# Performance work log

Hardware: AMD Instinct MI355X
Metric: run time of the kernel (lower is better)

The kernel has to match this reference:

```python
import jax, jax.numpy as jnp
import numpy as np

PS = 16          # patch size
NFREQ = 2        # PatchExtractor Fourier frequencies -> 4 + 8*F = 20 channels
E = 8            # num experts
CAP_FACTOR = 1.25


def _pos_feats(h, w, ps, F=NFREQ, dtype=jnp.float32):
    """Fourier positional features per patch pixel: [h*w, 4+8F, ps, ps]."""
    H, W = h * ps, w * ps
    r = jnp.arange(h, dtype=dtype)
    c = jnp.arange(w, dtype=dtype)
    i = jnp.arange(ps, dtype=dtype)
    j = jnp.arange(ps, dtype=dtype)
    gy = (r[:, None, None, None] * ps + i[None, None, :, None]) / H
    gx = (c[None, :, None, None] * ps + j[None, None, None, :]) / W
    pcy = (r[:, None, None, None] + 0.5) / h
    pcx = (c[None, :, None, None] + 0.5) / w
    gy, gx, pcy, pcx = [jnp.broadcast_to(t, (h, w, ps, ps)) for t in (gy, gx, pcy, pcx)]
    feats = [gx, gy, pcx, pcy]
    for f in range(F):
        s = (2.0 ** f) * 2.0 * jnp.pi
        for t in (gx, gy, pcx, pcy):
            feats += [jnp.sin(s * t), jnp.cos(s * t)]
    out = jnp.stack(feats, 0)                       # [4+8F, h, w, ps, ps]
    return out.transpose(1, 2, 0, 3, 4).reshape(h * w, 4 + 8 * F, ps, ps)


def setup_inputs() -> dict:
    key = jax.random.key(0)
    ks = jax.random.split(key, 5)
    X = jax.random.normal(ks[0], (16, 3, 256, 256), jnp.float32)
    expert_w = jax.random.normal(ks[1], (E, 8, 3, 3, 3), jnp.float32) * 0.1   # [E, Cout, Cin, kh, kw]
    expert_b = jnp.zeros((E, 8), jnp.float32)
    gate_w = jax.random.normal(ks[2], (E, 23), jnp.float32) * 0.1             # 1x1 gate conv, mean-pooled
    gate_b = jnp.zeros((E,), jnp.float32)
    lin_w = jax.random.normal(ks[3], (512, 1000), jnp.float32) * 0.02
    lin_b = jnp.zeros((1000,), jnp.float32)
    return dict(X=X, expert_w=expert_w, expert_b=expert_b, gate_w=gate_w,
                gate_b=gate_b, lin_w=lin_w, lin_b=lin_b)


def reference(X, expert_w, expert_b, gate_w, gate_b, lin_w, lin_b):
    B, C, H, W = X.shape
    h, w = H // PS, W // PS
    P = h * w
    N = B * P
    Ccap = int(np.ceil(N * CAP_FACTOR / E))

    # 1. patch extraction: [B,C,H,W] -> [N, C, ps, ps]
    Xp = X.reshape(B, C, h, PS, w, PS).transpose(0, 2, 4, 1, 3, 5).reshape(N, C, PS, PS)

    # patch coords = patch pixels + Fourier positional channels -> [N, C+20, ps, ps]
    pos = _pos_feats(h, w, PS, dtype=X.dtype)
    coords = jnp.concatenate([Xp, jnp.tile(pos, (B, 1, 1, 1))], axis=1)

    # 2. router: 1x1 conv + global mean pool -> logits [N, E]; top-1 capacity routing
    logits = jnp.einsum('nchw,ec->ne', coords, gate_w) / (PS * PS) + gate_b
    probs = jax.nn.softmax(logits, axis=-1)
    e_idx = jnp.argmax(probs, axis=-1)                         # [N] expert choice
    one_hot = jax.nn.one_hot(e_idx, E, dtype=jnp.int32)
    c_idx = jnp.sum(jnp.cumsum(one_hot, axis=0) * one_hot, axis=-1) - 1  # rank within expert
    valid = c_idx < Ccap
    gates = jnp.take_along_axis(probs, e_idx[:, None], axis=1)[:, 0] * valid.astype(probs.dtype)

    # 3. dispatch: scatter patches into per-expert capacity buffers (slot Ccap = dump)
    slot = jnp.where(valid, c_idx, Ccap)
    buf = jnp.zeros((E, Ccap + 1, C, PS, PS), X.dtype).at[e_idx, slot].set(Xp)
    expert_in = buf[:, :Ccap]                                  # [E, Ccap, C, ps, ps]

    # 4. per-expert conv 3x3 + bias + ReLU
    def run_expert(inp, wgt, b):
        y = jax.lax.conv_general_dilated(inp, wgt, (1, 1), 'SAME')
        return jax.nn.relu(y + b[None, :, None, None])

    yout = jax.vmap(run_expert)(expert_in, expert_w, expert_b)  # [E, Ccap, Cout, ps, ps]
    Cout = yout.shape[2]

    # 5. combine: gather each patch's expert output, weighted by gate
    out_n = gates[:, None, None, None] * yout[e_idx, jnp.minimum(c_idx, Ccap - 1)]

    # reassemble patches into full image
    img = out_n.reshape(B, h, w, Cout, PS, PS).transpose(0, 3, 1, 4, 2, 5).reshape(B, Cout, H, W)

    # switch-style aux loss: E * sum_e f_e * p_e
    f_e = jnp.mean(one_hot.astype(probs.dtype) * valid[:, None].astype(probs.dtype), axis=0)
    p_e = jnp.mean(probs, axis=0)
    aux_loss = E * jnp.sum(f_e * p_e)

    # head: adaptive avg pool to 8x8, flatten, linear
    pooled = img.reshape(B, Cout, 8, H // 8, 8, W // 8).mean(axis=(3, 5))
    feat = pooled.reshape(B, -1)
    logits_cls = feat @ lin_w + lin_b
    return logits_cls, aux_loss
```

## Files before the change

kernel.cpp:

```cpp
#include <hip/hip_runtime.h>
#include <math.h>

#define CCAP 640
#define TWO_PI 6.28318530717958647692f

__global__ __launch_bounds__(256) void k_fused(const float* __restrict__ X,
        const float* __restrict__ gw, const float* __restrict__ gb,
        const float* __restrict__ ew, const float* __restrict__ eb,
        int* __restrict__ eidx, float* __restrict__ ptop,
        float* __restrict__ pspart, float* __restrict__ snc)
{
    int tid = threadIdx.x;
    int wave = tid >> 6, lane = tid & 63;
    int n = blockIdx.x * 4 + wave;
    int b = n >> 8, p = n & 255, pr = p >> 4, pc = p & 15;
    int i = lane >> 2, q = lane & 3;

    __shared__ float pb[4][8];

    float4 px[3];
    #pragma unroll
    for (int c = 0; c < 3; ++c)
        px[c] = *(const float4*)(X +
            ((size_t)(b * 3 + c) * 256 + pr * 16 + i) * 256 + pc * 16 + q * 4);

    float S0, S1, S2;
    {
        float s0 = (px[0].x + px[0].y) + (px[0].z + px[0].w);
        float s1 = (px[1].x + px[1].y) + (px[1].z + px[1].w);
        float s2 = (px[2].x + px[2].y) + (px[2].z + px[2].w);
        #pragma unroll
        for (int off = 1; off < 64; off <<= 1) {
            s0 += __shfl_xor(s0, off, 64);
            s1 += __shfl_xor(s1, off, 64);
            s2 += __shfl_xor(s2, off, 64);
        }
        S0 = s0; S1 = s1; S2 = s2;
    }

    int m = lane & 15;
    float tx = (float)(pc * 16 + m) * (1.0f / 256.0f);
    float ty = (float)(pr * 16 + m) * (1.0f / 256.0f);
    float t0 = __sinf(TWO_PI * tx),       t1 = __cosf(TWO_PI * tx);
    float t2 = __sinf(2.f * TWO_PI * tx), t3 = __cosf(2.f * TWO_PI * tx);
    float t4 = __sinf(TWO_PI * ty),       t5 = __cosf(TWO_PI * ty);
    float t6 = __sinf(2.f * TWO_PI * ty), t7 = __cosf(2.f * TWO_PI * ty);
    #pragma unroll
    for (int off = 1; off < 16; off <<= 1) {
        t0 += __shfl_xor(t0, off, 64);  t1 += __shfl_xor(t1, off, 64);
        t2 += __shfl_xor(t2, off, 64);  t3 += __shfl_xor(t3, off, 64);
        t4 += __shfl_xor(t4, off, 64);  t5 += __shfl_xor(t5, off, 64);
        t6 += __shfl_xor(t6, off, 64);  t7 += __shfl_xor(t7, off, 64);
    }

    float pcx = ((float)pc + 0.5f) * (1.0f / 16.0f);
    float pcy = ((float)pr + 0.5f) * (1.0f / 16.0f);
    float S[23];
    S[0] = S0; S[1] = S1; S[2] = S2;
    S[3] = 16.f * ((float)pc + 0.46875f);
    S[4] = 16.f * ((float)pr + 0.46875f);
    S[5] = 256.f * pcx;  S[6] = 256.f * pcy;
    S[7]  = 16.f * t0;  S[8]  = 16.f * t1;
    S[9]  = 16.f * t4;  S[10] = 16.f * t5;
    S[11] = 256.f * __sinf(TWO_PI * pcx);  S[12] = 256.f * __cosf(TWO_PI * pcx);
    S[13] = 256.f * __sinf(TWO_PI * pcy);  S[14] = 256.f * __cosf(TWO_PI * pcy);
    S[15] = 16.f * t2;  S[16] = 16.f * t3;
    S[17] = 16.f * t6;  S[18] = 16.f * t7;
    S[19] = 256.f * __sinf(2.f * TWO_PI * pcx);  S[20] = 256.f * __cosf(2.f * TWO_PI * pcx);
    S[21] = 256.f * __sinf(2.f * TWO_PI * pcy);  S[22] = 256.f * __cosf(2.f * TWO_PI * pcy);

    float lg[8];
    float mx = -1e30f;
    #pragma unroll
    for (int ee = 0; ee < 8; ++ee) {
        float a = 0.f;
        #pragma unroll
        for (int c = 0; c < 23; ++c) a += S[c] * gw[ee * 23 + c];
        lg[ee] = a * (1.0f / 256.0f) + gb[ee];
        mx = fmaxf(mx, lg[ee]);
    }
    float den = 0.f;
    float prob[8];
    #pragma unroll
    for (int ee = 0; ee < 8; ++ee) { prob[ee] = __expf(lg[ee] - mx); den += prob[ee]; }
    float inv = 1.0f / den;
    #pragma unroll
    for (int ee = 0; ee < 8; ++ee) prob[ee] *= inv;
    int am = 0; float best = lg[0];
    #pragma unroll
    for (int ee = 1; ee < 8; ++ee) if (lg[ee] > best) { best = lg[ee]; am = ee; }

    int e = __builtin_amdgcn_readfirstlane(am);
    const float* wp = ew + (size_t)e * 216;

    float acc[8][4];
    #pragma unroll
    for (int co = 0; co < 8; ++co) {
        float bv = eb[e * 8 + co];
        #pragma unroll
        for (int k = 0; k < 4; ++k) acc[co][k] = bv;
    }

    #pragma unroll
    for (int ci = 0; ci < 3; ++ci) {
        float4 v = px[ci];
        float own[6];
        own[1] = v.x; own[2] = v.y; own[3] = v.z; own[4] = v.w;
        float L = __shfl(v.w, lane - 1, 64);
        float R = __shfl(v.x, lane + 1, 64);
        own[0] = (q == 0) ? 0.f : L;
        own[5] = (q == 3) ? 0.f : R;
        float up[6], dn[6];
        #pragma unroll
        for (int c6 = 0; c6 < 6; ++c6) {
            float u = __shfl(own[c6], lane - 4, 64);
            float d = __shfl(own[c6], lane + 4, 64);
            up[c6] = (i == 0)  ? 0.f : u;
            dn[c6] = (i == 15) ? 0.f : d;
        }
        #pragma unroll
        for (int co = 0; co < 8; ++co) {
            const float* w9 = wp + co * 27 + ci * 9;
            float w0 = w9[0], w1 = w9[1], w2 = w9[2];
            float w3 = w9[3], w4 = w9[4], w5 = w9[5];
            float w6 = w9[6], w7 = w9[7], w8 = w9[8];
            #pragma unroll
            for (int k = 0; k < 4; ++k) {
                float a = acc[co][k];
                a += up[k]  * w0 + up[k + 1]  * w1 + up[k + 2]  * w2;
                a += own[k] * w3 + own[k + 1] * w4 + own[k + 2] * w5;
                a += dn[k]  * w6 + dn[k + 1]  * w7 + dn[k + 2]  * w8;
                acc[co][k] = a;
            }
        }
    }

    float sum8[8];
    #pragma unroll
    for (int co = 0; co < 8; ++co) {
        float v = fmaxf(acc[co][0], 0.f) + fmaxf(acc[co][1], 0.f)
                + fmaxf(acc[co][2], 0.f) + fmaxf(acc[co][3], 0.f);
        #pragma unroll
        for (int off = 1; off < 64; off <<= 1) v += __shfl_xor(v, off, 64);
        sum8[co] = v;
    }

    float outv = sum8[0];
    #pragma unroll
    for (int co = 1; co < 8; ++co) outv = (lane == co) ? sum8[co] : outv;
    float pv = prob[0];
    #pragma unroll
    for (int ee = 1; ee < 8; ++ee) pv = (lane == ee) ? prob[ee] : pv;
    float tp = prob[0];
    #pragma unroll
    for (int ee = 1; ee < 8; ++ee) tp = (am == ee) ? prob[ee] : tp;

    if (lane < 8) {
        snc[(size_t)n * 8 + lane] = outv;
        pb[wave][lane] = pv;
    }
    if (lane == 0) { eidx[n] = am; ptop[n] = tp; }
    __syncthreads();
    if (tid < 8)
        pspart[(size_t)blockIdx.x * 8 + tid] =
            pb[0][tid] + pb[1][tid] + pb[2][tid] + pb[3][tid];
}

__global__ __launch_bounds__(256) void k_cls(const int* __restrict__ eidx,
        const float* __restrict__ ptop, const float* __restrict__ pspart,
        const float* __restrict__ snc, const float* __restrict__ lw,
        const float* __restrict__ lb, float* __restrict__ out,
        float* __restrict__ out_aux)
{
    int b = blockIdx.x;
    int chunk = blockIdx.y;
    int t = threadIdx.x;
    int wave = t >> 6, lane = t & 63;

    __shared__ float gl[4096];
    __shared__ float feat[512];
    __shared__ unsigned long long wlo[4], whi[4];
    __shared__ float part[64][4];
    __shared__ float pred[4][8];

    unsigned long long lo = 0ull, hi = 0ull;
    int myE[16];
    #pragma unroll
    for (int k4 = 0; k4 < 4; ++k4) {
        int4 v = ((const int4*)eidx)[t * 4 + k4];
        myE[k4 * 4 + 0] = v.x; myE[k4 * 4 + 1] = v.y;
        myE[k4 * 4 + 2] = v.z; myE[k4 * 4 + 3] = v.w;
    }
    #pragma unroll
    for (int k = 0; k < 16; ++k) {
        int e = myE[k];
        int sh = 16 * (e & 3);
        if (e < 4) lo += 1ull << sh; else hi += 1ull << sh;
    }

    unsigned long long slo = lo, shi = hi;
    #pragma unroll
    for (int off = 1; off < 64; off <<= 1) {
        unsigned long long a = __shfl_up(slo, off, 64);
        unsigned long long c = __shfl_up(shi, off, 64);
        if (lane >= off) { slo += a; shi += c; }
    }
    if (lane == 63) { wlo[wave] = slo; whi[wave] = shi; }
    __syncthreads();

    unsigned long long plo = 0ull, phi = 0ull;
    #pragma unroll
    for (int w2 = 0; w2 < 4; ++w2)
        if (w2 < wave) { plo += wlo[w2]; phi += whi[w2]; }
    unsigned long long elo = plo + (slo - lo);
    unsigned long long ehi = phi + (shi - hi);

    #pragma unroll
    for (int k = 0; k < 16; ++k) {
        int nn = t * 16 + k;
        int e = myE[k];
        int sh = 16 * (e & 3);
        unsigned long long cur = (e < 4) ? elo : ehi;
        int r = (int)((cur >> sh) & 0xFFFFull);
        gl[nn] = (r < CCAP) ? ptop[nn] : 0.0f;
        unsigned long long inc = 1ull << sh;
        if (e < 4) elo += inc; else ehi += inc;
    }
    __syncthreads();

    for (int f = t; f < 512; f += 256) {
        int co = f >> 6, rem = f & 63, py = rem >> 3, pxx = rem & 7;
        float sum = 0.f;
        #pragma unroll
        for (int dy = 0; dy < 2; ++dy)
            #pragma unroll
            for (int dx = 0; dx < 2; ++dx) {
                int nn = b * 256 + (2 * py + dy) * 16 + (2 * pxx + dx);
                sum += gl[nn] * snc[(size_t)nn * 8 + co];
            }
        feat[f] = sum * (1.0f / 1024.0f);
    }
    __syncthreads();

    int c = t & 63, quarter = t >> 6;
    int kk = chunk * 64 + c;
    int kcl = (kk > 999) ? 999 : kk;
    float acc = 0.f;
    const float* lp = lw + (size_t)(quarter * 128) * 1000 + kcl;
    const float* fp = feat + quarter * 128;
    #pragma unroll 8
    for (int f2 = 0; f2 < 128; ++f2) acc += fp[f2] * lp[(size_t)f2 * 1000];
    part[c][quarter] = acc;
    __syncthreads();
    if (t < 64) {
        int ko = chunk * 64 + t;
        if (ko < 1000)
            out[b * 1000 + ko] =
                part[t][0] + part[t][1] + part[t][2] + part[t][3] + lb[ko];
    }

    if (b == 0 && chunk == 0) {
        float lp8[8] = {0.f, 0.f, 0.f, 0.f, 0.f, 0.f, 0.f, 0.f};
        for (int r = t; r < 1024; r += 256) {
            const float4* p4 = (const float4*)(pspart + (size_t)r * 8);
            float4 a = p4[0], d = p4[1];
            lp8[0] += a.x; lp8[1] += a.y; lp8[2] += a.z; lp8[3] += a.w;
            lp8[4] += d.x; lp8[5] += d.y; lp8[6] += d.z; lp8[7] += d.w;
        }
        #pragma unroll
        for (int ee = 0; ee < 8; ++ee) {
            float v = lp8[ee];
            #pragma unroll
            for (int off = 1; off < 64; off <<= 1) v += __shfl_xor(v, off, 64);
            lp8[ee] = v;
        }
        if (lane == 0) {
            #pragma unroll
            for (int ee = 0; ee < 8; ++ee) pred[wave][ee] = lp8[ee];
        }
        __syncthreads();
        if (t == 0) {
            unsigned long long tl = wlo[0] + wlo[1] + wlo[2] + wlo[3];
            unsigned long long th = whi[0] + whi[1] + whi[2] + whi[3];
            float aux = 0.f;
            #pragma unroll
            for (int ee = 0; ee < 8; ++ee) {
                int tot = (ee < 4) ? (int)((tl >> (16 * ee)) & 0xFFFFull)
                                   : (int)((th >> (16 * (ee - 4))) & 0xFFFFull);
                float fe = (float)min(tot, CCAP) * (1.0f / 4096.0f);
                float pe = (pred[0][ee] + pred[1][ee] + pred[2][ee] + pred[3][ee])
                           * (1.0f / 4096.0f);
                aux += fe * pe;
            }
            out_aux[0] = 8.0f * aux;
        }
    }
}

extern "C" void kernel_launch(void* const* d_in, const int* in_sizes, int n_in,
                              void* d_out, int out_size, void* d_ws, size_t ws_size,
                              hipStream_t stream) {
    const float* X  = (const float*)d_in[0];
    const float* ew = (const float*)d_in[1];
    const float* eb = (const float*)d_in[2];
    const float* gw = (const float*)d_in[3];
    const float* gb = (const float*)d_in[4];
    const float* lw = (const float*)d_in[5];
    const float* lb = (const float*)d_in[6];
    float* out = (float*)d_out;

    char* ws = (char*)d_ws;
    int*   eidx   = (int*)  (ws + 0);
    float* ptop   = (float*)(ws + 16384);
    float* pspart = (float*)(ws + 32768);
    float* snc    = (float*)(ws + 65536);

    k_fused<<<1024, 256, 0, stream>>>(X, gw, gb, ew, eb, eidx, ptop, pspart, snc);
    k_cls<<<dim3(16, 16), 256, 0, stream>>>(eidx, ptop, pspart, snc, lw, lb,
                                            out, out + 16000);
}
```

Measured before the change: 102.9 us.

## Merge gate/conv and classifier kernels into one cooperative launch with grid sync

Replaces the two-kernel sequence with a single cooperative kernel of 512 blocks, where each wave handles two patches, then a grid-wide sync hands off to the routing/pool/classifier stage run by 256 blocks. The goal is to remove the second kernel launch and its inter-kernel gap. Per-block prob partials are now 512 rows instead of 1024. In exchange it adds a grid barrier, an occupancy query on every launch, and cooperative-launch overhead, and it keeps the old two-kernel path as a fallback.

```diff
diff --git a/kernel.cpp b/kernel.cpp
--- a/kernel.cpp
+++ b/kernel.cpp
@@ -1,22 +1,20 @@
 #include <hip/hip_runtime.h>
+#include <hip/hip_cooperative_groups.h>
 #include <math.h>
+
+namespace cg = cooperative_groups;
 
 #define CCAP 640
 #define TWO_PI 6.28318530717958647692f
 
-__global__ __launch_bounds__(256) void k_fused(const float* __restrict__ X,
-        const float* __restrict__ gw, const float* __restrict__ gb,
-        const float* __restrict__ ew, const float* __restrict__ eb,
-        int* __restrict__ eidx, float* __restrict__ ptop,
-        float* __restrict__ pspart, float* __restrict__ snc)
+__device__ __forceinline__ void patch_gate_conv(
+        const float* __restrict__ X,  const float* __restrict__ gw,
+        const float* __restrict__ gb, const float* __restrict__ ew,
+        const float* __restrict__ eb, int n, int lane,
+        float& outv, float& pv, float& tp, int& am_out)
 {
-    int tid = threadIdx.x;
-    int wave = tid >> 6, lane = tid & 63;
-    int n = blockIdx.x * 4 + wave;
     int b = n >> 8, p = n & 255, pr = p >> 4, pc = p & 15;
     int i = lane >> 2, q = lane & 3;
-
-    __shared__ float pb[4][8];
 
     float4 px[3];
     #pragma unroll
@@ -145,43 +143,31 @@
         sum8[co] = v;
     }
 
-    float outv = sum8[0];
-    #pragma unroll
-    for (int co = 1; co < 8; ++co) outv = (lane == co) ? sum8[co] : outv;
-    float pv = prob[0];
-    #pragma unroll
-    for (int ee = 1; ee < 8; ++ee) pv = (lane == ee) ? prob[ee] : pv;
-    float tp = prob[0];
-    #pragma unroll
-    for (int ee = 1; ee < 8; ++ee) tp = (am == ee) ? prob[ee] : tp;
-
-    if (lane < 8) {
-        snc[(size_t)n * 8 + lane] = outv;
-        pb[wave][lane] = pv;
-    }
-    if (lane == 0) { eidx[n] = am; ptop[n] = tp; }
-    __syncthreads();
-    if (tid < 8)
-        pspart[(size_t)blockIdx.x * 8 + tid] =
-            pb[0][tid] + pb[1][tid] + pb[2][tid] + pb[3][tid];
-}
-
-__global__ __launch_bounds__(256) void k_cls(const int* __restrict__ eidx,
-        const float* __restrict__ ptop, const float* __restrict__ pspart,
-        const float* __restrict__ snc, const float* __restrict__ lw,
-        const float* __restrict__ lb, float* __restrict__ out,
-        float* __restrict__ out_aux)
+    float ov = sum8[0];
+    #pragma unroll
+    for (int co = 1; co < 8; ++co) ov = (lane == co) ? sum8[co] : ov;
+    float pvv = prob[0];
+    #pragma unroll
+    for (int ee = 1; ee < 8; ++ee) pvv = (lane == ee) ? prob[ee] : pvv;
+    float tpv = prob[0];
+    #pragma unroll
+    for (int ee = 1; ee < 8; ++ee) tpv = (am == ee) ? prob[ee] : tpv;
+
+    outv = ov; pv = pvv; tp = tpv; am_out = am;
+}
+
+__device__ __forceinline__ void route_pool_cls(
+        const int* __restrict__ eidx, const float* __restrict__ ptop,
+        const float* __restrict__ pspart, const float* __restrict__ snc,
+        const float* __restrict__ lw, const float* __restrict__ lb,
+        float* __restrict__ out, float* __restrict__ out_aux,
+        int bid, int t, int psrows,
+        float* gl, float* feat, unsigned long long* wlo,
+        unsigned long long* whi, float (*part)[4], float (*pred)[8])
 {
-    int b = blockIdx.x;
-    int chunk = blockIdx.y;
-    int t = threadIdx.x;
+    int b = bid >> 4;
+    int chunk = bid & 15;
     int wave = t >> 6, lane = t & 63;
-
-    __shared__ float gl[4096];
-    __shared__ float feat[512];
-    __shared__ unsigned long long wlo[4], whi[4];
-    __shared__ float part[64][4];
-    __shared__ float pred[4][8];
 
     unsigned long long lo = 0ull, hi = 0ull;
     int myE[16];
@@ -259,9 +245,9 @@
                 part[t][0] + part[t][1] + part[t][2] + part[t][3] + lb[ko];
     }
 
-    if (b == 0 && chunk == 0) {
+    if (bid == 0) {
         float lp8[8] = {0.f, 0.f, 0.f, 0.f, 0.f, 0.f, 0.f, 0.f};
-        for (int r = t; r < 1024; r += 256) {
+        for (int r = t; r < psrows; r += 256) {
             const float4* p4 = (const float4*)(pspart + (size_t)r * 8);
             float4 a = p4[0], d = p4[1];
             lp8[0] += a.x; lp8[1] += a.y; lp8[2] += a.z; lp8[3] += a.w;
@@ -297,6 +283,94 @@
     }
 }
 
+__global__ __launch_bounds__(256, 2) void k_all_coop(
+        const float* __restrict__ X,  const float* __restrict__ gw,
+        const float* __restrict__ gb, const float* __restrict__ ew,
+        const float* __restrict__ eb, const float* __restrict__ lw,
+        const float* __restrict__ lb, int* __restrict__ eidx,
+        float* __restrict__ ptop, float* __restrict__ pspart,
+        float* __restrict__ snc, float* __restrict__ out,
+        float* __restrict__ out_aux)
+{
+    int tid = threadIdx.x;
+    int wave = tid >> 6, lane = tid & 63;
+
+    __shared__ float pb[4][8];
+    __shared__ float gl[4096];
+    __shared__ float feat[512];
+    __shared__ unsigned long long wlo[4], whi[4];
+    __shared__ float part[64][4];
+    __shared__ float pred[4][8];
+
+    {
+        float pvacc = 0.f;
+        #pragma unroll
+        for (int k = 0; k < 2; ++k) {
+            int n = blockIdx.x * 8 + wave * 2 + k;
+            float outv, pv, tp; int am;
+            patch_gate_conv(X, gw, gb, ew, eb, n, lane, outv, pv, tp, am);
+            if (lane < 8) snc[(size_t)n * 8 + lane] = outv;
+            if (lane == 0) { eidx[n] = am; ptop[n] = tp; }
+            pvacc += pv;
+        }
+        if (lane < 8) pb[wave][lane] = pvacc;
+        __syncthreads();
+        if (tid < 8)
+            pspart[(size_t)blockIdx.x * 8 + tid] =
+                pb[0][tid] + pb[1][tid] + pb[2][tid] + pb[3][tid];
+    }
+
+    __threadfence();
+    cg::this_grid().sync();
+    if (blockIdx.x >= 256) return;
+
+    route_pool_cls(eidx, ptop, pspart, snc, lw, lb, out, out_aux,
+                   blockIdx.x, tid, 512, gl, feat, wlo, whi, part, pred);
+}
+
+__global__ __launch_bounds__(256) void k_fused(const float* __restrict__ X,
+        const float* __restrict__ gw, const float* __restrict__ gb,
+        const float* __restrict__ ew, const float* __restrict__ eb,
+        int* __restrict__ eidx, float* __restrict__ ptop,
+        float* __restrict__ pspart, float* __restrict__ snc)
+{
+    int tid = threadIdx.x;
+    int wave = tid >> 6, lane = tid & 63;
+    int n = blockIdx.x * 4 + wave;
+
+    __shared__ float pb[4][8];
+
+    float outv, pv, tp; int am;
+    patch_gate_conv(X, gw, gb, ew, eb, n, lane, outv, pv, tp, am);
+
+    if (lane < 8) {
+        snc[(size_t)n * 8 + lane] = outv;
+        pb[wave][lane] = pv;
+    }
+    if (lane == 0) { eidx[n] = am; ptop[n] = tp; }
+    __syncthreads();
+    if (tid < 8)
+        pspart[(size_t)blockIdx.x * 8 + tid] =
+            pb[0][tid] + pb[1][tid] + pb[2][tid] + pb[3][tid];
+}
+
+__global__ __launch_bounds__(256) void k_cls(const int* __restrict__ eidx,
+        const float* __restrict__ ptop, const float* __restrict__ pspart,
+        const float* __restrict__ snc, const float* __restrict__ lw,
+        const float* __restrict__ lb, float* __restrict__ out,
+        float* __restrict__ out_aux)
+{
+    __shared__ float gl[4096];
+    __shared__ float feat[512];
+    __shared__ unsigned long long wlo[4], whi[4];
+    __shared__ float part[64][4];
+    __shared__ float pred[4][8];
+
+    int bid = blockIdx.x * 16 + blockIdx.y;
+    route_pool_cls(eidx, ptop, pspart, snc, lw, lb, out, out_aux,
+                   bid, threadIdx.x, 1024, gl, feat, wlo, whi, part, pred);
+}
+
 extern "C" void kernel_launch(void* const* d_in, const int* in_sizes, int n_in,
                               void* d_out, int out_size, void* d_ws, size_t ws_size,
                               hipStream_t stream) {
@@ -308,6 +382,7 @@
     const float* lw = (const float*)d_in[5];
     const float* lb = (const float*)d_in[6];
     float* out = (float*)d_out;
+    float* out_aux = out + 16000;
 
     char* ws = (char*)d_ws;
     int*   eidx   = (int*)  (ws + 0);
@@ -315,7 +390,24 @@
     float* pspart = (float*)(ws + 32768);
     float* snc    = (float*)(ws + 65536);
 
+    int maxB = 0;
+    hipError_t qe = hipOccupancyMaxActiveBlocksPerMultiprocessor(
+        &maxB, (const void*)k_all_coop, 256, 0);
+    bool coop = (qe == hipSuccess && maxB >= 2);
+
+    if (coop) {
+        void* args[] = { (void*)&X, (void*)&gw, (void*)&gb, (void*)&ew,
+                         (void*)&eb, (void*)&lw, (void*)&lb, (void*)&eidx,
+                         (void*)&ptop, (void*)&pspart, (void*)&snc,
+                         (void*)&out, (void*)&out_aux };
+        hipError_t le = hipLaunchCooperativeKernel((const void*)k_all_coop,
+                                                   dim3(512), dim3(256),
+                                                   args, 0, stream);
+        if (le == hipSuccess) return;
+        (void)hipGetLastError();
+    }
+
     k_fused<<<1024, 256, 0, stream>>>(X, gw, gb, ew, eb, eidx, ptop, pspart, snc);
     k_cls<<<dim3(16, 16), 256, 0, stream>>>(eidx, ptop, pspart, snc, lw, lb,
-                                            out, out + 16000);
-}
+                                            out, out_aux);
+}
```

Result: no change. 102.5 us (-0.4%).
